# Kernel tuning notes

Hardware: AMD Instinct MI355X
Metric: run time of the kernel (lower is better)

## Reference

```python
import jax, jax.numpy as jnp
import numpy as np

B, S, D = 16, 4096, 128
LN_EPS = 1e-5
REC_EPS = 1e-8


def setup_inputs() -> dict:
    key = jax.random.key(0)
    k1, k2, k3, k4 = jax.random.split(key, 4)
    return {
        "C": jax.random.normal(k1, (B, S, D), dtype=jnp.float32),
        "V": jax.random.normal(k2, (B, S, D), dtype=jnp.float32),
        "W": jax.random.normal(k3, (B, S, D), dtype=jnp.float32),
        "encoder_context": jax.random.normal(k4, (B, D), dtype=jnp.float32),
        "time_modulation": jnp.full((1, 1, D), 0.5, dtype=jnp.float32),
        "context_modulation": jnp.full((1, D), 0.5, dtype=jnp.float32),
        "ln_weight": jnp.ones((D,), dtype=jnp.float32),
        "ln_bias": jnp.zeros((D,), dtype=jnp.float32),
    }


def reference(C, V, W, encoder_context, time_modulation, context_modulation, ln_weight, ln_bias):
    b_, s_, d_ = C.shape
    tm = time_modulation[0, 0]  # [D]
    # context gate is time-invariant: compute once
    ctx_add = jax.nn.sigmoid(encoder_context * context_modulation) * encoder_context  # [B,D]

    def step(carry, xs):
        a, bst = carry  # a: [B,1], bst: [B,D]
        c_t, v_t, w_t = xs  # each [B,D]
        decay = jax.nn.sigmoid(w_t * tm)  # [B,D]
        ec = jnp.exp(c_t)  # [B,D]
        a = decay.mean(axis=1, keepdims=True) * a + ec.sum(axis=1, keepdims=True)
        bst = decay * bst + ec * v_t + ctx_add
        out_t = bst / (a + REC_EPS)
        return (a, bst), out_t

    a0 = jnp.zeros((b_, 1), dtype=C.dtype)
    b0 = jnp.zeros((b_, d_), dtype=C.dtype)
    xs = (jnp.swapaxes(C, 0, 1), jnp.swapaxes(V, 0, 1), jnp.swapaxes(W, 0, 1))  # [S,B,D]
    _, ys = jax.lax.scan(step, (a0, b0), xs)  # ys: [S,B,D]
    res = jnp.swapaxes(ys, 0, 1)  # [B,S,D]

    mu = jnp.mean(res, axis=-1, keepdims=True)
    var = jnp.var(res, axis=-1, keepdims=True)
    normed = (res - mu) * jax.lax.rsqrt(var + LN_EPS)
    return normed * ln_weight + ln_bias
```

## Files before the change

### kernel.cpp

```cpp
#include <hip/hip_runtime.h>

#define BB   16
#define SS   4096
#define DD   128
#define NCH  256
#define TT   (SS / NCH)
#define GPB  4
#define NTHR 128

#define LN_EPS  1e-5f
#define REC_EPS 1e-8f

__device__ __forceinline__ float fast_rcp(float x) { return __builtin_amdgcn_rcpf(x); }
__device__ __forceinline__ float sigm(float x) { return fast_rcp(1.0f + __expf(-x)); }

__device__ __forceinline__ void red2(float& a, float& b) {
#pragma unroll
    for (int m = 16; m >= 1; m >>= 1) {
        a += __shfl_xor(a, m, 64);
        b += __shfl_xor(b, m, 64);
    }
}

__global__ __launch_bounds__(NTHR) void pass1_kernel(
    const float* __restrict__ C, const float* __restrict__ V, const float* __restrict__ W,
    const float* __restrict__ enc, const float* __restrict__ tmod, const float* __restrict__ cmod,
    float* __restrict__ Pbuf, float* __restrict__ Qbuf,
    float* __restrict__ PaBuf, float* __restrict__ QaBuf,
    float* __restrict__ mbuf, float* __restrict__ ebuf)
{
    const int grp  = threadIdx.x >> 5;
    const int lane = threadIdx.x & 31;
    const int gc   = blockIdx.x * GPB + grp;
    const int b    = gc >> 8;
    const int ch   = gc & (NCH - 1);
    const int d4   = lane << 2;

    const float4 tm = *(const float4*)(tmod + d4);
    const float4 cm = *(const float4*)(cmod + d4);
    const float4 ec = *(const float4*)(enc + b * DD + d4);
    float4 ctx;
    ctx.x = sigm(ec.x * cm.x) * ec.x;
    ctx.y = sigm(ec.y * cm.y) * ec.y;
    ctx.z = sigm(ec.z * cm.z) * ec.z;
    ctx.w = sigm(ec.w * cm.w) * ec.w;

    float4 P = make_float4(1.f, 1.f, 1.f, 1.f);
    float4 Q = make_float4(0.f, 0.f, 0.f, 0.f);
    float pa = 1.f, qa = 0.f;

    const int t0 = ch * TT;
    const size_t base = ((size_t)b * SS + t0) * DD + d4;
    const float4* Cp = (const float4*)(C + base);
    const float4* Vp = (const float4*)(V + base);
    const float4* Wp = (const float4*)(W + base);

#pragma unroll 4
    for (int t = 0; t < TT; ++t) {
        const float4 c4 = Cp[t * (DD / 4)];
        const float4 v4 = Vp[t * (DD / 4)];
        const float4 w4 = Wp[t * (DD / 4)];
        float4 dec, e4;
        dec.x = sigm(w4.x * tm.x); dec.y = sigm(w4.y * tm.y);
        dec.z = sigm(w4.z * tm.z); dec.w = sigm(w4.w * tm.w);
        e4.x = __expf(c4.x); e4.y = __expf(c4.y);
        e4.z = __expf(c4.z); e4.w = __expf(c4.w);

        Q.x = dec.x * Q.x + (e4.x * v4.x + ctx.x);
        Q.y = dec.y * Q.y + (e4.y * v4.y + ctx.y);
        Q.z = dec.z * Q.z + (e4.z * v4.z + ctx.z);
        Q.w = dec.w * Q.w + (e4.w * v4.w + ctx.w);
        P.x *= dec.x; P.y *= dec.y; P.z *= dec.z; P.w *= dec.w;

        float sd = (dec.x + dec.y) + (dec.z + dec.w);
        float se = (e4.x + e4.y) + (e4.z + e4.w);
        red2(sd, se);
        const float mt = sd * (1.0f / DD);
        pa *= mt;
        qa = mt * qa + se;
        if (lane == 0) {
            mbuf[(size_t)b * SS + t0 + t] = mt;
            ebuf[(size_t)b * SS + t0 + t] = se;
        }
    }

    *(float4*)(Pbuf + (size_t)gc * DD + d4) = P;
    *(float4*)(Qbuf + (size_t)gc * DD + d4) = Q;
    if (lane == 0) { PaBuf[gc] = pa; QaBuf[gc] = qa; }
}

__global__ __launch_bounds__(NCH) void pass2_kernel(
    const float* __restrict__ Pbuf, const float* __restrict__ Qbuf,
    const float* __restrict__ PaBuf, const float* __restrict__ QaBuf,
    float* __restrict__ bst0, float* __restrict__ a0)
{
    const int b = blockIdx.x;
    const int tid = threadIdx.x;
    __shared__ float sP[NCH], sQ[NCH];

    float p = PaBuf[b * NCH + tid];
    float q = QaBuf[b * NCH + tid];
#pragma unroll
    for (int off = 1; off < NCH; off <<= 1) {
        sP[tid] = p; sQ[tid] = q;
        __syncthreads();
        if (tid >= off) {
            const float pp = sP[tid - off], qq = sQ[tid - off];
            q = p * qq + q;
            p = p * pp;
        }
        __syncthreads();
    }
    sQ[tid] = q;
    __syncthreads();
    a0[b * NCH + tid] = (tid == 0) ? 0.f : sQ[tid - 1];

    if (tid < DD) {
        float s = 0.f;
#pragma unroll 8
        for (int ch = 0; ch < NCH; ++ch) {
            const size_t idx = ((size_t)b * NCH + ch) * DD + tid;
            bst0[idx] = s;
            s = Pbuf[idx] * s + Qbuf[idx];
        }
    }
}

__global__ __launch_bounds__(NTHR) void pass3_kernel(
    const float* __restrict__ C, const float* __restrict__ V, const float* __restrict__ W,
    const float* __restrict__ enc, const float* __restrict__ tmod, const float* __restrict__ cmod,
    const float* __restrict__ lnw, const float* __restrict__ lnb,
    const float* __restrict__ bst0, const float* __restrict__ a0,
    const float* __restrict__ mbuf, const float* __restrict__ ebuf,
    float* __restrict__ out)
{
    const int grp  = threadIdx.x >> 5;
    const int lane = threadIdx.x & 31;
    const int gc   = blockIdx.x * GPB + grp;
    const int b    = gc >> 8;
    const int ch   = gc & (NCH - 1);
    const int d4   = lane << 2;

    const float4 tm = *(const float4*)(tmod + d4);
    const float4 cm = *(const float4*)(cmod + d4);
    const float4 ec = *(const float4*)(enc + b * DD + d4);
    float4 ctx;
    ctx.x = sigm(ec.x * cm.x) * ec.x;
    ctx.y = sigm(ec.y * cm.y) * ec.y;
    ctx.z = sigm(ec.z * cm.z) * ec.z;
    ctx.w = sigm(ec.w * cm.w) * ec.w;
    const float4 gw = *(const float4*)(lnw + d4);
    const float4 gb = *(const float4*)(lnb + d4);

    float4 bst = *(const float4*)(bst0 + (size_t)gc * DD + d4);
    float a = a0[gc];

    const int t0 = ch * TT;
    const size_t base = ((size_t)b * SS + t0) * DD + d4;
    const float4* Cp = (const float4*)(C + base);
    const float4* Vp = (const float4*)(V + base);
    const float4* Wp = (const float4*)(W + base);
    float4* Op = (float4*)(out + base);
    const float* mp = mbuf + (size_t)b * SS + t0;
    const float* ep = ebuf + (size_t)b * SS + t0;

#pragma unroll 2
    for (int t = 0; t < TT; ++t) {
        const float4 c4 = Cp[t * (DD / 4)];
        const float4 v4 = Vp[t * (DD / 4)];
        const float4 w4 = Wp[t * (DD / 4)];
        const float mt = mp[t];
        const float et = ep[t];

        float4 dec, e4;
        dec.x = sigm(w4.x * tm.x); dec.y = sigm(w4.y * tm.y);
        dec.z = sigm(w4.z * tm.z); dec.w = sigm(w4.w * tm.w);
        e4.x = __expf(c4.x); e4.y = __expf(c4.y);
        e4.z = __expf(c4.z); e4.w = __expf(c4.w);

        a = mt * a + et;
        bst.x = dec.x * bst.x + (e4.x * v4.x + ctx.x);
        bst.y = dec.y * bst.y + (e4.y * v4.y + ctx.y);
        bst.z = dec.z * bst.z + (e4.z * v4.z + ctx.z);
        bst.w = dec.w * bst.w + (e4.w * v4.w + ctx.w);

        const float inva = fast_rcp(a + REC_EPS);
        float4 o;
        o.x = bst.x * inva; o.y = bst.y * inva;
        o.z = bst.z * inva; o.w = bst.w * inva;

        float s1 = (o.x + o.y) + (o.z + o.w);
        float s2 = (o.x * o.x + o.y * o.y) + (o.z * o.z + o.w * o.w);
        red2(s1, s2);
        const float mu  = s1 * (1.0f / DD);
        const float var = s2 * (1.0f / DD) - mu * mu;
        const float rs  = rsqrtf(var + LN_EPS);

        float4 r;
        r.x = (o.x - mu) * rs * gw.x + gb.x;
        r.y = (o.y - mu) * rs * gw.y + gb.y;
        r.z = (o.z - mu) * rs * gw.z + gb.z;
        r.w = (o.w - mu) * rs * gw.w + gb.w;
        Op[t * (DD / 4)] = r;
    }
}

extern "C" void kernel_launch(void* const* d_in, const int* in_sizes, int n_in,
                              void* d_out, int out_size, void* d_ws, size_t ws_size,
                              hipStream_t stream)
{
    const float* C    = (const float*)d_in[0];
    const float* V    = (const float*)d_in[1];
    const float* W    = (const float*)d_in[2];
    const float* enc  = (const float*)d_in[3];
    const float* tmod = (const float*)d_in[4];
    const float* cmod = (const float*)d_in[5];
    const float* lnw  = (const float*)d_in[6];
    const float* lnb  = (const float*)d_in[7];
    float* out = (float*)d_out;

    float* ws    = (float*)d_ws;
    float* Pbuf  = ws;
    float* Qbuf  = Pbuf  + (size_t)BB * NCH * DD;
    float* bst0  = Qbuf  + (size_t)BB * NCH * DD;
    float* mbuf  = bst0  + (size_t)BB * NCH * DD;
    float* ebuf  = mbuf  + (size_t)BB * SS;
    float* PaBuf = ebuf  + (size_t)BB * SS;
    float* QaBuf = PaBuf + (size_t)BB * NCH;
    float* a0Buf = QaBuf + (size_t)BB * NCH;

    const int nblk = BB * NCH / GPB;
    pass1_kernel<<<nblk, NTHR, 0, stream>>>(C, V, W, enc, tmod, cmod,
                                            Pbuf, Qbuf, PaBuf, QaBuf, mbuf, ebuf);
    pass2_kernel<<<BB, NCH, 0, stream>>>(Pbuf, Qbuf, PaBuf, QaBuf, bst0, a0Buf);
    pass3_kernel<<<nblk, NTHR, 0, stream>>>(C, V, W, enc, tmod, cmod, lnw, lnb,
                                            bst0, a0Buf, mbuf, ebuf, out);
}
```

Before: 179.2 us.

## Cache decay and exp as packed bf16 pair and parallelize chunk-carry scan

Pass 1 now writes the decay and exp(C) values for every element as two bf16 halves packed into one 32-bit word. Pass 3 reads that word in place of both C and W, which removes one input stream and the sigmoid/exp work from the final pass but adds a full-size write in pass 1. The per-dimension carry scan in pass 2 becomes a two-level scan over 128 blocks instead of 16 serial threads per batch, which should shorten that latency-bound stage. The bf16 rounding of decay and exp lowers precision in the recurrence and could push the output past tolerance.

```diff
diff --git a/kernel.cpp b/kernel.cpp
--- a/kernel.cpp
+++ b/kernel.cpp
@@ -8,11 +8,23 @@
 #define GPB  4
 #define NTHR 128
 
+#define DT   16
+#define SUBS 16
+#define CPS  (NCH / SUBS)
+
 #define LN_EPS  1e-5f
 #define REC_EPS 1e-8f
 
 __device__ __forceinline__ float fast_rcp(float x) { return __builtin_amdgcn_rcpf(x); }
 __device__ __forceinline__ float sigm(float x) { return fast_rcp(1.0f + __expf(-x)); }
+
+__device__ __forceinline__ unsigned pack_de(float d, float e) {
+    unsigned ud = (__float_as_uint(d) + 0x8000u) >> 16;
+    unsigned ue = (__float_as_uint(e) + 0x8000u) & 0xFFFF0000u;
+    return ue | ud;
+}
+__device__ __forceinline__ float de_lo(unsigned u) { return __uint_as_float(u << 16); }
+__device__ __forceinline__ float de_hi(unsigned u) { return __uint_as_float(u & 0xFFFF0000u); }
 
 __device__ __forceinline__ void red2(float& a, float& b) {
 #pragma unroll
@@ -25,6 +37,7 @@
 __global__ __launch_bounds__(NTHR) void pass1_kernel(
     const float* __restrict__ C, const float* __restrict__ V, const float* __restrict__ W,
     const float* __restrict__ enc, const float* __restrict__ tmod, const float* __restrict__ cmod,
+    unsigned* __restrict__ DE,
     float* __restrict__ Pbuf, float* __restrict__ Qbuf,
     float* __restrict__ PaBuf, float* __restrict__ QaBuf,
     float* __restrict__ mbuf, float* __restrict__ ebuf)
@@ -54,6 +67,7 @@
     const float4* Cp = (const float4*)(C + base);
     const float4* Vp = (const float4*)(V + base);
     const float4* Wp = (const float4*)(W + base);
+    uint4* DEp = (uint4*)(DE + base);
 
 #pragma unroll 4
     for (int t = 0; t < TT; ++t) {
@@ -66,6 +80,11 @@
         e4.x = __expf(c4.x); e4.y = __expf(c4.y);
         e4.z = __expf(c4.z); e4.w = __expf(c4.w);
 
+        uint4 u;
+        u.x = pack_de(dec.x, e4.x); u.y = pack_de(dec.y, e4.y);
+        u.z = pack_de(dec.z, e4.z); u.w = pack_de(dec.w, e4.w);
+        DEp[t * (DD / 4)] = u;
+
         Q.x = dec.x * Q.x + (e4.x * v4.x + ctx.x);
         Q.y = dec.y * Q.y + (e4.y * v4.y + ctx.y);
         Q.z = dec.z * Q.z + (e4.z * v4.z + ctx.z);
@@ -89,46 +108,75 @@
     if (lane == 0) { PaBuf[gc] = pa; QaBuf[gc] = qa; }
 }
 
-__global__ __launch_bounds__(NCH) void pass2_kernel(
+__global__ __launch_bounds__(256) void pass2_kernel(
     const float* __restrict__ Pbuf, const float* __restrict__ Qbuf,
     const float* __restrict__ PaBuf, const float* __restrict__ QaBuf,
     float* __restrict__ bst0, float* __restrict__ a0)
 {
-    const int b = blockIdx.x;
+    const int b   = blockIdx.x >> 3;
+    const int dt  = blockIdx.x & 7;
     const int tid = threadIdx.x;
-    __shared__ float sP[NCH], sQ[NCH];
-
-    float p = PaBuf[b * NCH + tid];
-    float q = QaBuf[b * NCH + tid];
-#pragma unroll
-    for (int off = 1; off < NCH; off <<= 1) {
-        sP[tid] = p; sQ[tid] = q;
+    const int dl  = tid & (DT - 1);
+    const int sub = tid >> 4;
+    const int d   = dt * DT + dl;
+
+    __shared__ float cP[SUBS][DT], cQ[SUBS][DT], ent[SUBS][DT];
+    __shared__ float sPa[NCH], sQa[NCH];
+
+    const int ch0 = sub * CPS;
+    const size_t base = ((size_t)b * NCH + ch0) * DD + d;
+    float Pr[CPS], Qr[CPS];
+    float p = 1.f, q = 0.f;
+#pragma unroll
+    for (int i = 0; i < CPS; ++i) {
+        Pr[i] = Pbuf[base + (size_t)i * DD];
+        Qr[i] = Qbuf[base + (size_t)i * DD];
+        q = Pr[i] * q + Qr[i];
+        p = Pr[i] * p;
+    }
+    cP[sub][dl] = p; cQ[sub][dl] = q;
+    __syncthreads();
+
+    if (tid < DT) {
+        float s = 0.f;
+#pragma unroll
+        for (int sb = 0; sb < SUBS; ++sb) {
+            ent[sb][tid] = s;
+            s = cP[sb][tid] * s + cQ[sb][tid];
+        }
+    }
+    __syncthreads();
+
+    float s = ent[sub][dl];
+#pragma unroll
+    for (int i = 0; i < CPS; ++i) {
+        bst0[base + (size_t)i * DD] = s;
+        s = Pr[i] * s + Qr[i];
+    }
+
+    if (dt == 0) {
+        float pa = PaBuf[b * NCH + tid];
+        float qa = QaBuf[b * NCH + tid];
+#pragma unroll
+        for (int off = 1; off < NCH; off <<= 1) {
+            sPa[tid] = pa; sQa[tid] = qa;
+            __syncthreads();
+            if (tid >= off) {
+                const float pp = sPa[tid - off], qq = sQa[tid - off];
+                qa = pa * qq + qa;
+                pa = pa * pp;
+            }
+            __syncthreads();
+        }
+        sQa[tid] = qa;
         __syncthreads();
-        if (tid >= off) {
-            const float pp = sP[tid - off], qq = sQ[tid - off];
-            q = p * qq + q;
-            p = p * pp;
-        }
-        __syncthreads();
-    }
-    sQ[tid] = q;
-    __syncthreads();
-    a0[b * NCH + tid] = (tid == 0) ? 0.f : sQ[tid - 1];
-
-    if (tid < DD) {
-        float s = 0.f;
-#pragma unroll 8
-        for (int ch = 0; ch < NCH; ++ch) {
-            const size_t idx = ((size_t)b * NCH + ch) * DD + tid;
-            bst0[idx] = s;
-            s = Pbuf[idx] * s + Qbuf[idx];
-        }
+        a0[b * NCH + tid] = (tid == 0) ? 0.f : sQa[tid - 1];
     }
 }
 
 __global__ __launch_bounds__(NTHR) void pass3_kernel(
-    const float* __restrict__ C, const float* __restrict__ V, const float* __restrict__ W,
-    const float* __restrict__ enc, const float* __restrict__ tmod, const float* __restrict__ cmod,
+    const float* __restrict__ V, const unsigned* __restrict__ DE,
+    const float* __restrict__ enc, const float* __restrict__ cmod,
     const float* __restrict__ lnw, const float* __restrict__ lnb,
     const float* __restrict__ bst0, const float* __restrict__ a0,
     const float* __restrict__ mbuf, const float* __restrict__ ebuf,
@@ -141,7 +189,6 @@
     const int ch   = gc & (NCH - 1);
     const int d4   = lane << 2;
 
-    const float4 tm = *(const float4*)(tmod + d4);
     const float4 cm = *(const float4*)(cmod + d4);
     const float4 ec = *(const float4*)(enc + b * DD + d4);
     float4 ctx;
@@ -157,32 +204,24 @@
 
     const int t0 = ch * TT;
     const size_t base = ((size_t)b * SS + t0) * DD + d4;
-    const float4* Cp = (const float4*)(C + base);
     const float4* Vp = (const float4*)(V + base);
-    const float4* Wp = (const float4*)(W + base);
+    const uint4*  DEp = (const uint4*)(DE + base);
     float4* Op = (float4*)(out + base);
     const float* mp = mbuf + (size_t)b * SS + t0;
     const float* ep = ebuf + (size_t)b * SS + t0;
 
-#pragma unroll 2
+#pragma unroll 4
     for (int t = 0; t < TT; ++t) {
-        const float4 c4 = Cp[t * (DD / 4)];
         const float4 v4 = Vp[t * (DD / 4)];
-        const float4 w4 = Wp[t * (DD / 4)];
+        const uint4  u  = DEp[t * (DD / 4)];
         const float mt = mp[t];
         const float et = ep[t];
 
-        float4 dec, e4;
-        dec.x = sigm(w4.x * tm.x); dec.y = sigm(w4.y * tm.y);
-        dec.z = sigm(w4.z * tm.z); dec.w = sigm(w4.w * tm.w);
-        e4.x = __expf(c4.x); e4.y = __expf(c4.y);
-        e4.z = __expf(c4.z); e4.w = __expf(c4.w);
-
         a = mt * a + et;
-        bst.x = dec.x * bst.x + (e4.x * v4.x + ctx.x);
-        bst.y = dec.y * bst.y + (e4.y * v4.y + ctx.y);
-        bst.z = dec.z * bst.z + (e4.z * v4.z + ctx.z);
-        bst.w = dec.w * bst.w + (e4.w * v4.w + ctx.w);
+        bst.x = de_lo(u.x) * bst.x + (de_hi(u.x) * v4.x + ctx.x);
+        bst.y = de_lo(u.y) * bst.y + (de_hi(u.y) * v4.y + ctx.y);
+        bst.z = de_lo(u.z) * bst.z + (de_hi(u.z) * v4.z + ctx.z);
+        bst.w = de_lo(u.w) * bst.w + (de_hi(u.w) * v4.w + ctx.w);
 
         const float inva = fast_rcp(a + REC_EPS);
         float4 o;
@@ -220,7 +259,8 @@
     float* out = (float*)d_out;
 
     float* ws    = (float*)d_ws;
-    float* Pbuf  = ws;
+    unsigned* DEbuf = (unsigned*)ws;
+    float* Pbuf  = ws    + (size_t)BB * SS * DD;
     float* Qbuf  = Pbuf  + (size_t)BB * NCH * DD;
     float* bst0  = Qbuf  + (size_t)BB * NCH * DD;
     float* mbuf  = bst0  + (size_t)BB * NCH * DD;
@@ -230,9 +270,9 @@
     float* a0Buf = QaBuf + (size_t)BB * NCH;
 
     const int nblk = BB * NCH / GPB;
-    pass1_kernel<<<nblk, NTHR, 0, stream>>>(C, V, W, enc, tmod, cmod,
+    pass1_kernel<<<nblk, NTHR, 0, stream>>>(C, V, W, enc, tmod, cmod, DEbuf,
                                             Pbuf, Qbuf, PaBuf, QaBuf, mbuf, ebuf);
-    pass2_kernel<<<BB, NCH, 0, stream>>>(Pbuf, Qbuf, PaBuf, QaBuf, bst0, a0Buf);
-    pass3_kernel<<<nblk, NTHR, 0, stream>>>(C, V, W, enc, tmod, cmod, lnw, lnb,
+    pass2_kernel<<<BB * 8, 256, 0, stream>>>(Pbuf, Qbuf, PaBuf, QaBuf, bst0, a0Buf);
+    pass3_kernel<<<nblk, NTHR, 0, stream>>>(V, DEbuf, enc, cmod, lnw, lnb,
                                             bst0, a0Buf, mbuf, ebuf, out);
 }
```

After: 162.7 us. 9.2% less time.
